# Performance work log

Measured on AMD Instinct MI355X. Metric: run time of the kernel, lower is better.

The kernel has to match this reference:

```python
import jax, jax.numpy as jnp
import numpy as np

POS_MARGIN = 0.01
NEG_MARGIN = 0.2
REG_WEIGHT = 0.1
N, D = 8192, 256
NUM_CLASSES = 512


def setup_inputs() -> dict:
    key = jax.random.key(0)
    k1, k2 = jax.random.split(key)
    embeds = jax.random.normal(k1, (N, D), dtype=jnp.float32)
    labels = jax.random.randint(k2, (N,), 0, NUM_CLASSES, dtype=jnp.int64)
    return {"embeds": embeds, "labels": labels}


def reference(embeds, labels):
    n, d = embeds.shape
    # L2-normalize embeddings (normalize_embeds=True)
    e = embeds / jnp.linalg.norm(embeds, axis=1, keepdims=True)

    # var(e_i - e_j, ddof=1) over feature dim, computed without the [N,N,D] tensor:
    # var = (D/(D-1)) * ( mean(e_i^2) + mean(e_j^2) - 2*mean(e_i*e_j) - (m_i - m_j)^2 )
    m = e.mean(axis=1)                      # [N]
    s = (e * e).mean(axis=1)                # [N]
    g = (e @ e.T) / d                       # [N,N] = mean(e_i * e_j) over D
    corr = d / (d - 1.0)
    var_diff = corr * (s[:, None] + s[None, :] - 2.0 * g - (m[:, None] - m[None, :]) ** 2)
    row_var = corr * (s - m * m)            # torch.var(e, dim=1), unbiased
    distmat = var_diff / row_var[:, None]

    same = labels[:, None] == labels[None, :]
    eye = jnp.eye(n, dtype=bool)
    pos_mask = same & (~eye)                # all same-label pairs (anchor != positive)
    neg_mask = ~same                        # all diff-label pairs

    pos_l = jax.nn.relu(distmat - POS_MARGIN) * pos_mask
    neg_l = jax.nn.relu(NEG_MARGIN - distmat) * neg_mask

    # avg_nonzero_only=True: sum / (# strictly-positive entries + 1e-12)
    pos_loss = pos_l.sum() / ((pos_l > 0).sum().astype(jnp.float32) + 1e-12)
    neg_loss = neg_l.sum() / ((neg_l > 0).sum().astype(jnp.float32) + 1e-12)

    loss = pos_loss + neg_loss
    loss = loss + jnp.abs(e.sum(axis=1)).mean() * REG_WEIGHT
    return loss
```

## Files before the change

kernel.cpp:

```cpp
#include <hip/hip_runtime.h>
#include <hip/hip_bf16.h>

#define NROWS 8192
#define DDIM 256
#define BT 128
#define BK 64
#define GT (NROWS / BT)
#define NBT (GT * (GT + 1) / 2)

using bf16x8 = __attribute__((ext_vector_type(8))) __bf16;
using f32x4  = __attribute__((ext_vector_type(4))) float;

__device__ __forceinline__ void glds16(const unsigned short* g, unsigned short* l) {
    __builtin_amdgcn_global_load_lds(
        (const __attribute__((address_space(1))) unsigned int*)g,
        (__attribute__((address_space(3))) unsigned int*)l,
        16, 0, 0);
}

__device__ __forceinline__ unsigned short f2bf(float f) {
    unsigned int b = __float_as_uint(f);
    unsigned int r = b + 0x7fffu + ((b >> 16) & 1u);
    return (unsigned short)(r >> 16);
}

__global__ __launch_bounds__(256) void rowstats_kernel(
    const float* __restrict__ x, unsigned short* __restrict__ ebf,
    float* __restrict__ aA, float* __restrict__ dA,
    float* __restrict__ bA, float* __restrict__ m2A,
    float* __restrict__ rabs)
{
    int wave = threadIdx.x >> 6;
    int lane = threadIdx.x & 63;
    int row  = blockIdx.x * 4 + wave;

    const float4 v = reinterpret_cast<const float4*>(x + (size_t)row * DDIM)[lane];
    float ss = v.x * v.x + v.y * v.y + v.z * v.z + v.w * v.w;
    float sm = v.x + v.y + v.z + v.w;
    #pragma unroll
    for (int off = 32; off >= 1; off >>= 1) {
        ss += __shfl_xor(ss, off);
        sm += __shfl_xor(sm, off);
    }
    float invn = 1.0f / sqrtf(ss);

    ushort4 o;
    o.x = f2bf(v.x * invn);
    o.y = f2bf(v.y * invn);
    o.z = f2bf(v.z * invn);
    o.w = f2bf(v.w * invn);
    reinterpret_cast<ushort4*>(ebf + (size_t)row * DDIM)[lane] = o;

    if (lane == 0) {
        float Se  = sm * invn;
        float Se2 = ss * invn * invn;
        float m = Se * (1.0f / DDIM);
        float s = Se2 * (1.0f / DDIM);
        float b = s - m * m;
        float a = 1.0f / b;
        aA[row]  = a;
        dA[row]  = a * m;
        bA[row]  = b;
        m2A[row] = 2.0f * m;
        rabs[row] = fabsf(Se);
    }
}

__global__ __launch_bounds__(256) void snr_gemm_kernel(
    const unsigned short* __restrict__ ebf,
    const float* __restrict__ aA, const float* __restrict__ dA,
    const float* __restrict__ bA, const float* __restrict__ m2A,
    const int* __restrict__ labels,
    float* __restrict__ partials)
{
    __shared__ __align__(16) unsigned short As[BT * BK];
    __shared__ __align__(16) unsigned short Bs[BT * BK];
    __shared__ float sAi[BT], sDi[BT], sBi[BT], sM2i[BT];
    __shared__ float sAj[BT], sDj[BT], sBj[BT], sM2j[BT];
    __shared__ int   sLi[BT], sLj[BT];
    __shared__ float redbuf[4][4];

    int tid  = threadIdx.x;
    int lane = tid & 63;
    int wave = tid >> 6;
    int wr = (wave >> 1) * 64;
    int wc = (wave & 1) * 64;

    int t = blockIdx.x;
    int bi = (int)((2.0f * GT + 1.0f
                    - sqrtf((2.0f * GT + 1.0f) * (2.0f * GT + 1.0f) - 8.0f * (float)t)) * 0.5f);
    while ((bi + 1) * GT - ((bi + 1) * bi) / 2 <= t) ++bi;
    while (bi * GT - (bi * (bi - 1)) / 2 > t) --bi;
    int bj = bi + (t - (bi * GT - (bi * (bi - 1)) / 2));
    int rowBase = bi * BT, colBase = bj * BT;
    bool diag = (bi == bj);

    if (tid < BT) {
        int gi = rowBase + tid;
        sAi[tid] = aA[gi]; sDi[tid] = dA[gi]; sBi[tid] = bA[gi]; sM2i[tid] = m2A[gi];
        sLi[tid] = labels[gi];
    } else {
        int tt = tid - BT;
        int gj = colBase + tt;
        sAj[tt] = aA[gj]; sDj[tt] = dA[gj]; sBj[tt] = bA[gj]; sM2j[tt] = m2A[gj];
        sLj[tt] = labels[gj];
    }

    const unsigned short* gA[4];
    const unsigned short* gB[4];
    unsigned short* lpA[4];
    unsigned short* lpB[4];
    #pragma unroll
    for (int p = 0; p < 4; ++p) {
        int q   = p * 256 + tid;
        int row = q >> 3;
        int kc  = (q & 7) ^ (row & 7);
        gA[p] = ebf + (size_t)(rowBase + row) * DDIM + kc * 8;
        gB[p] = ebf + (size_t)(colBase + row) * DDIM + kc * 8;
        lpA[p] = As + q * 8;
        lpB[p] = Bs + q * 8;
    }

    int mrow = lane & 15;
    int kch  = lane >> 4;
    int offA[4][2], offB[4][2];
    #pragma unroll
    for (int t4 = 0; t4 < 4; ++t4) {
        int rA = wr + t4 * 16 + mrow;
        int rB = wc + t4 * 16 + mrow;
        #pragma unroll
        for (int h = 0; h < 2; ++h) {
            offA[t4][h] = (rA * 8 + ((h * 4 + kch) ^ (rA & 7))) * 8;
            offB[t4][h] = (rB * 8 + ((h * 4 + kch) ^ (rB & 7))) * 8;
        }
    }

    f32x4 acc[4][4];
    #pragma unroll
    for (int a = 0; a < 4; ++a)
        #pragma unroll
        for (int b = 0; b < 4; ++b)
            acc[a][b] = (f32x4){0.f, 0.f, 0.f, 0.f};

    for (int it = 0; it < 4; ++it) {
        #pragma unroll
        for (int p = 0; p < 4; ++p) {
            glds16(gA[p], lpA[p]);
            glds16(gB[p], lpB[p]);
            gA[p] += BK;
            gB[p] += BK;
        }
        asm volatile("s_waitcnt vmcnt(0)" ::: "memory");
        __syncthreads();

        #pragma unroll
        for (int h = 0; h < 2; ++h) {
            bf16x8 aF[4], bF[4];
            #pragma unroll
            for (int t4 = 0; t4 < 4; ++t4) {
                aF[t4] = *reinterpret_cast<const bf16x8*>(As + offA[t4][h]);
                bF[t4] = *reinterpret_cast<const bf16x8*>(Bs + offB[t4][h]);
            }
            #pragma unroll
            for (int ti = 0; ti < 4; ++ti)
                #pragma unroll
                for (int tj = 0; tj < 4; ++tj)
                    acc[ti][tj] = __builtin_amdgcn_mfma_f32_16x16x32_bf16(aF[ti], bF[tj], acc[ti][tj], 0, 0, 0);
        }
        __syncthreads();
    }

    float ps = 0.f, ns = 0.f;
    unsigned int pcw = 0, ncw = 0;
    int subr = (lane >> 4) * 4;
    int cj   = lane & 15;

    float bCj[4], mCj[4], aCj[4], dCj[4];
    int LCj[4];
    #pragma unroll
    for (int tj = 0; tj < 4; ++tj) {
        int lj = wc + tj * 16 + cj;
        bCj[tj] = sBj[lj]; mCj[tj] = sM2j[lj];
        aCj[tj] = sAj[lj]; dCj[tj] = sDj[lj];
        LCj[tj] = sLj[lj];
    }

    if (!diag) {
        #pragma unroll
        for (int ti = 0; ti < 4; ++ti) {
            #pragma unroll
            for (int r = 0; r < 4; ++r) {
                int li = wr + ti * 16 + subr + r;
                float aR = sAi[li], dR = sDi[li], bR = sBi[li], m2R = sM2i[li];
                int LR = sLi[li];
                #pragma unroll
                for (int tj = 0; tj < 4; ++tj) {
                    float g2 = acc[ti][tj][r] * (1.0f / 128.0f);
                    bool same = (LR == LCj[tj]);
                    float dij = fmaf(aR, bCj[tj] - g2, fmaf(dR, mCj[tj], 1.0f));
                    float dji = fmaf(aCj[tj], bR - g2, fmaf(dCj[tj], m2R, 1.0f));
                    float v1 = same ? (dij - 0.01f) : (0.2f - dij);
                    float v2 = same ? (dji - 0.01f) : (0.2f - dji);
                    bool p1 = same && (v1 > 0.f);
                    bool p2 = same && (v2 > 0.f);
                    bool n1 = (!same) && (v1 > 0.f);
                    bool n2 = (!same) && (v2 > 0.f);
                    ps += (p1 ? v1 : 0.f) + (p2 ? v2 : 0.f);
                    ns += (n1 ? v1 : 0.f) + (n2 ? v2 : 0.f);
                    pcw += (unsigned)__popcll(__ballot(p1)) + (unsigned)__popcll(__ballot(p2));
                    ncw += (unsigned)__popcll(__ballot(n1)) + (unsigned)__popcll(__ballot(n2));
                }
            }
        }
    } else {
        #pragma unroll
        for (int ti = 0; ti < 4; ++ti) {
            #pragma unroll
            for (int r = 0; r < 4; ++r) {
                int li = wr + ti * 16 + subr + r;
                float aR = sAi[li], dR = sDi[li];
                int LR = sLi[li];
                #pragma unroll
                for (int tj = 0; tj < 4; ++tj) {
                    int lj = wc + tj * 16 + cj;
                    float g2 = acc[ti][tj][r] * (1.0f / 128.0f);
                    bool same = (LR == LCj[tj]);
                    float dij = fmaf(aR, bCj[tj] - g2, fmaf(dR, mCj[tj], 1.0f));
                    float v1 = same ? (dij - 0.01f) : (0.2f - dij);
                    bool p1 = same && (li != lj) && (v1 > 0.f);
                    bool n1 = (!same) && (v1 > 0.f);
                    ps += p1 ? v1 : 0.f;
                    ns += n1 ? v1 : 0.f;
                    pcw += (unsigned)__popcll(__ballot(p1));
                    ncw += (unsigned)__popcll(__ballot(n1));
                }
            }
        }
    }

    #pragma unroll
    for (int off = 32; off >= 1; off >>= 1) {
        ps += __shfl_down(ps, off);
        ns += __shfl_down(ns, off);
    }
    if (lane == 0) {
        redbuf[wave][0] = ps; redbuf[wave][1] = ns;
        redbuf[wave][2] = (float)pcw; redbuf[wave][3] = (float)ncw;
    }
    __syncthreads();
    if (tid < 4) {
        float v = redbuf[0][tid] + redbuf[1][tid] + redbuf[2][tid] + redbuf[3][tid];
        partials[blockIdx.x * 4 + tid] = v;
    }
}

__global__ __launch_bounds__(256) void finalize_kernel(
    const float* __restrict__ partials, const float* __restrict__ rabs,
    float* __restrict__ out)
{
    int tid = threadIdx.x;
    float s0 = 0, s1 = 0, s2 = 0, s3 = 0, rr = 0;
    for (int i = tid; i < NBT; i += 256) {
        float4 p = reinterpret_cast<const float4*>(partials)[i];
        s0 += p.x; s1 += p.y; s2 += p.z; s3 += p.w;
    }
    for (int i = tid; i < NROWS; i += 256) rr += rabs[i];

    #pragma unroll
    for (int off = 32; off >= 1; off >>= 1) {
        s0 += __shfl_down(s0, off);
        s1 += __shfl_down(s1, off);
        s2 += __shfl_down(s2, off);
        s3 += __shfl_down(s3, off);
        rr += __shfl_down(rr, off);
    }
    __shared__ float red[4][5];
    int wave = tid >> 6, lane = tid & 63;
    if (lane == 0) {
        red[wave][0] = s0; red[wave][1] = s1; red[wave][2] = s2;
        red[wave][3] = s3; red[wave][4] = rr;
    }
    __syncthreads();
    if (tid == 0) {
        float a0 = 0, a1 = 0, a2 = 0, a3 = 0, a4 = 0;
        #pragma unroll
        for (int w = 0; w < 4; ++w) {
            a0 += red[w][0]; a1 += red[w][1]; a2 += red[w][2];
            a3 += red[w][3]; a4 += red[w][4];
        }
        float pos = a0 / (a2 + 1e-12f);
        float neg = a1 / (a3 + 1e-12f);
        out[0] = pos + neg + a4 * (0.1f / (float)NROWS);
    }
}

extern "C" void kernel_launch(void* const* d_in, const int* in_sizes, int n_in,
                              void* d_out, int out_size, void* d_ws, size_t ws_size,
                              hipStream_t stream) {
    const float* embeds = (const float*)d_in[0];
    const int*   labels = (const int*)d_in[1];
    float* out = (float*)d_out;

    char* ws = (char*)d_ws;
    unsigned short* ebf = (unsigned short*)ws;
    float* aA   = (float*)(ws + (size_t)NROWS * DDIM * 2);
    float* dA   = aA + NROWS;
    float* bA   = dA + NROWS;
    float* m2A  = bA + NROWS;
    float* rabs = m2A + NROWS;
    float* partials = rabs + NROWS;

    rowstats_kernel<<<NROWS / 4, 256, 0, stream>>>(embeds, ebf, aA, dA, bA, m2A, rabs);

    snr_gemm_kernel<<<NBT, 256, 0, stream>>>(ebf, aA, dA, bA, m2A, labels, partials);

    finalize_kernel<<<1, 256, 0, stream>>>(partials, rabs, out);
}
```

Baseline: 127.5 us.

## Mean-center embeddings, drop labels from GEMM epilogue, correct same-label pairs separately

Rowstats now stores mean-centered bf16 embeddings and folds the scale and offset terms into three per-row constants. The GEMM epilogue then treats every pair as a negative, needing one fma, a max and a count per element, with no label compares or ballots. A new per-class kernel recomputes same-label pairs with wave-level dot products, subtracts their negative contribution and adds their positive loss. Diagonal tiles also skip loading the B tile. The cost is an extra launch, a serial per-class pair loop capped at 512 rows per class, and the risk that bf16 dot products in the correction do not match the MFMA results exactly.

```diff
diff --git a/kernel.cpp b/kernel.cpp
--- a/kernel.cpp
+++ b/kernel.cpp
@@ -1,5 +1,4 @@
 #include <hip/hip_runtime.h>
-#include <hip/hip_bf16.h>
 
 #define NROWS 8192
 #define DDIM 256
@@ -7,6 +6,7 @@
 #define BK 64
 #define GT (NROWS / BT)
 #define NBT (GT * (GT + 1) / 2)
+#define NCLS 512
 
 using bf16x8 = __attribute__((ext_vector_type(8))) __bf16;
 using f32x4  = __attribute__((ext_vector_type(4))) float;
@@ -23,12 +23,14 @@
     unsigned int r = b + 0x7fffu + ((b >> 16) & 1u);
     return (unsigned short)(r >> 16);
 }
+__device__ __forceinline__ float bf2f(unsigned short u) {
+    return __uint_as_float((unsigned)u << 16);
+}
 
 __global__ __launch_bounds__(256) void rowstats_kernel(
     const float* __restrict__ x, unsigned short* __restrict__ ebf,
-    float* __restrict__ aA, float* __restrict__ dA,
-    float* __restrict__ bA, float* __restrict__ m2A,
-    float* __restrict__ rabs)
+    float* __restrict__ aP, float* __restrict__ bs,
+    float* __restrict__ cA, float* __restrict__ rabs)
 {
     int wave = threadIdx.x >> 6;
     int lane = threadIdx.x & 63;
@@ -43,42 +45,39 @@
         sm += __shfl_xor(sm, off);
     }
     float invn = 1.0f / sqrtf(ss);
+    float m = sm * invn * (1.0f / DDIM);
 
     ushort4 o;
-    o.x = f2bf(v.x * invn);
-    o.y = f2bf(v.y * invn);
-    o.z = f2bf(v.z * invn);
-    o.w = f2bf(v.w * invn);
+    o.x = f2bf(v.x * invn - m);
+    o.y = f2bf(v.y * invn - m);
+    o.z = f2bf(v.z * invn - m);
+    o.w = f2bf(v.w * invn - m);
     reinterpret_cast<ushort4*>(ebf + (size_t)row * DDIM)[lane] = o;
 
     if (lane == 0) {
-        float Se  = sm * invn;
-        float Se2 = ss * invn * invn;
-        float m = Se * (1.0f / DDIM);
-        float s = Se2 * (1.0f / DDIM);
-        float b = s - m * m;
-        float a = 1.0f / b;
-        aA[row]  = a;
-        dA[row]  = a * m;
-        bA[row]  = b;
-        m2A[row] = 2.0f * m;
-        rabs[row] = fabsf(Se);
+        float s  = ss * invn * invn * (1.0f / DDIM);
+        float b  = s - m * m;
+        float a  = 1.0f / b;
+        float ap = a * (1.0f / 128.0f);
+        float bv = -128.0f * b;
+        aP[row]   = ap;
+        bs[row]   = bv;
+        cA[row]   = fmaf(ap, bv, 0.2f);
+        rabs[row] = fabsf(sm * invn);
     }
 }
 
 __global__ __launch_bounds__(256) void snr_gemm_kernel(
     const unsigned short* __restrict__ ebf,
-    const float* __restrict__ aA, const float* __restrict__ dA,
-    const float* __restrict__ bA, const float* __restrict__ m2A,
-    const int* __restrict__ labels,
+    const float* __restrict__ aP, const float* __restrict__ bs,
+    const float* __restrict__ cA,
     float* __restrict__ partials)
 {
     __shared__ __align__(16) unsigned short As[BT * BK];
     __shared__ __align__(16) unsigned short Bs[BT * BK];
-    __shared__ float sAi[BT], sDi[BT], sBi[BT], sM2i[BT];
-    __shared__ float sAj[BT], sDj[BT], sBj[BT], sM2j[BT];
-    __shared__ int   sLi[BT], sLj[BT];
-    __shared__ float redbuf[4][4];
+    __shared__ float sAPi[BT], sBsi[BT], sCi[BT];
+    __shared__ float sAPj[BT], sBsj[BT], sCj[BT];
+    __shared__ float redbuf[4][2];
 
     int tid  = threadIdx.x;
     int lane = tid & 63;
@@ -97,13 +96,11 @@
 
     if (tid < BT) {
         int gi = rowBase + tid;
-        sAi[tid] = aA[gi]; sDi[tid] = dA[gi]; sBi[tid] = bA[gi]; sM2i[tid] = m2A[gi];
-        sLi[tid] = labels[gi];
+        sAPi[tid] = aP[gi]; sBsi[tid] = bs[gi]; sCi[tid] = cA[gi];
     } else {
         int tt = tid - BT;
         int gj = colBase + tt;
-        sAj[tt] = aA[gj]; sDj[tt] = dA[gj]; sBj[tt] = bA[gj]; sM2j[tt] = m2A[gj];
-        sLj[tt] = labels[gj];
+        sAPj[tt] = aP[gj]; sBsj[tt] = bs[gj]; sCj[tt] = cA[gj];
     }
 
     const unsigned short* gA[4];
@@ -142,13 +139,20 @@
         for (int b = 0; b < 4; ++b)
             acc[a][b] = (f32x4){0.f, 0.f, 0.f, 0.f};
 
+    const unsigned short* Bfrag = diag ? &As[0] : &Bs[0];
+
     for (int it = 0; it < 4; ++it) {
         #pragma unroll
         for (int p = 0; p < 4; ++p) {
             glds16(gA[p], lpA[p]);
-            glds16(gB[p], lpB[p]);
             gA[p] += BK;
-            gB[p] += BK;
+        }
+        if (!diag) {
+            #pragma unroll
+            for (int p = 0; p < 4; ++p) {
+                glds16(gB[p], lpB[p]);
+                gB[p] += BK;
+            }
         }
         asm volatile("s_waitcnt vmcnt(0)" ::: "memory");
         __syncthreads();
@@ -159,7 +163,7 @@
             #pragma unroll
             for (int t4 = 0; t4 < 4; ++t4) {
                 aF[t4] = *reinterpret_cast<const bf16x8*>(As + offA[t4][h]);
-                bF[t4] = *reinterpret_cast<const bf16x8*>(Bs + offB[t4][h]);
+                bF[t4] = *reinterpret_cast<const bf16x8*>(Bfrag + offB[t4][h]);
             }
             #pragma unroll
             for (int ti = 0; ti < 4; ++ti)
@@ -170,69 +174,58 @@
         __syncthreads();
     }
 
-    float ps = 0.f, ns = 0.f;
-    unsigned int pcw = 0, ncw = 0;
     int subr = (lane >> 4) * 4;
     int cj   = lane & 15;
 
-    float bCj[4], mCj[4], aCj[4], dCj[4];
-    int LCj[4];
+    float aPC[4], bsC[4], cC[4];
     #pragma unroll
     for (int tj = 0; tj < 4; ++tj) {
         int lj = wc + tj * 16 + cj;
-        bCj[tj] = sBj[lj]; mCj[tj] = sM2j[lj];
-        aCj[tj] = sAj[lj]; dCj[tj] = sDj[lj];
-        LCj[tj] = sLj[lj];
-    }
+        aPC[tj] = sAPj[lj]; bsC[tj] = sBsj[lj]; cC[tj] = sCj[lj];
+    }
+
+    float S = 0.f;
+    unsigned C = 0u;
 
     if (!diag) {
         #pragma unroll
         for (int ti = 0; ti < 4; ++ti) {
+            float aPR[4], bsR[4], cR[4];
             #pragma unroll
             for (int r = 0; r < 4; ++r) {
                 int li = wr + ti * 16 + subr + r;
-                float aR = sAi[li], dR = sDi[li], bR = sBi[li], m2R = sM2i[li];
-                int LR = sLi[li];
+                aPR[r] = sAPi[li]; bsR[r] = sBsi[li]; cR[r] = sCi[li];
+            }
+            #pragma unroll
+            for (int tj = 0; tj < 4; ++tj) {
                 #pragma unroll
-                for (int tj = 0; tj < 4; ++tj) {
-                    float g2 = acc[ti][tj][r] * (1.0f / 128.0f);
-                    bool same = (LR == LCj[tj]);
-                    float dij = fmaf(aR, bCj[tj] - g2, fmaf(dR, mCj[tj], 1.0f));
-                    float dji = fmaf(aCj[tj], bR - g2, fmaf(dCj[tj], m2R, 1.0f));
-                    float v1 = same ? (dij - 0.01f) : (0.2f - dij);
-                    float v2 = same ? (dji - 0.01f) : (0.2f - dji);
-                    bool p1 = same && (v1 > 0.f);
-                    bool p2 = same && (v2 > 0.f);
-                    bool n1 = (!same) && (v1 > 0.f);
-                    bool n2 = (!same) && (v2 > 0.f);
-                    ps += (p1 ? v1 : 0.f) + (p2 ? v2 : 0.f);
-                    ns += (n1 ? v1 : 0.f) + (n2 ? v2 : 0.f);
-                    pcw += (unsigned)__popcll(__ballot(p1)) + (unsigned)__popcll(__ballot(p2));
-                    ncw += (unsigned)__popcll(__ballot(n1)) + (unsigned)__popcll(__ballot(n2));
+                for (int r = 0; r < 4; ++r) {
+                    float raw = acc[ti][tj][r];
+                    float v1 = fmaf(aPR[r], raw + bsC[tj], cR[r]);
+                    float v2 = fmaf(aPC[tj], raw + bsR[r], cC[tj]);
+                    S += fmaxf(v1, 0.f) + fmaxf(v2, 0.f);
+                    C += (v1 > 0.f);
+                    C += (v2 > 0.f);
                 }
             }
         }
     } else {
         #pragma unroll
         for (int ti = 0; ti < 4; ++ti) {
+            float aPR[4], cR[4];
             #pragma unroll
             for (int r = 0; r < 4; ++r) {
                 int li = wr + ti * 16 + subr + r;
-                float aR = sAi[li], dR = sDi[li];
-                int LR = sLi[li];
+                aPR[r] = sAPi[li]; cR[r] = sCi[li];
+            }
+            #pragma unroll
+            for (int tj = 0; tj < 4; ++tj) {
                 #pragma unroll
-                for (int tj = 0; tj < 4; ++tj) {
-                    int lj = wc + tj * 16 + cj;
-                    float g2 = acc[ti][tj][r] * (1.0f / 128.0f);
-                    bool same = (LR == LCj[tj]);
-                    float dij = fmaf(aR, bCj[tj] - g2, fmaf(dR, mCj[tj], 1.0f));
-                    float v1 = same ? (dij - 0.01f) : (0.2f - dij);
-                    bool p1 = same && (li != lj) && (v1 > 0.f);
-                    bool n1 = (!same) && (v1 > 0.f);
-                    ps += p1 ? v1 : 0.f;
-                    ns += n1 ? v1 : 0.f;
-                    pcw += (unsigned)__popcll(__ballot(p1));
-                    ncw += (unsigned)__popcll(__ballot(n1));
+                for (int r = 0; r < 4; ++r) {
+                    float raw = acc[ti][tj][r];
+                    float v1 = fmaf(aPR[r], raw + bsC[tj], cR[r]);
+                    S += fmaxf(v1, 0.f);
+                    C += (v1 > 0.f);
                 }
             }
         }
@@ -240,57 +233,127 @@
 
     #pragma unroll
     for (int off = 32; off >= 1; off >>= 1) {
-        ps += __shfl_down(ps, off);
-        ns += __shfl_down(ns, off);
-    }
+        S += __shfl_down(S, off);
+        C += __shfl_down(C, off);
+    }
+    if (lane == 0) { redbuf[wave][0] = S; redbuf[wave][1] = (float)C; }
+    __syncthreads();
+    if (tid < 2) {
+        partials[blockIdx.x * 2 + tid] =
+            redbuf[0][tid] + redbuf[1][tid] + redbuf[2][tid] + redbuf[3][tid];
+    }
+}
+
+__global__ __launch_bounds__(256) void corr_kernel(
+    const unsigned short* __restrict__ ebf,
+    const float* __restrict__ aP, const float* __restrict__ bs,
+    const int* __restrict__ labels,
+    float* __restrict__ corr)
+{
+    __shared__ int rowsL[512];
+    __shared__ int cntS;
+    __shared__ float cred[4][4];
+    int tid  = threadIdx.x;
+    int lane = tid & 63;
+    int wave = tid >> 6;
+    int L = blockIdx.x;
+
+    if (tid == 0) cntS = 0;
+    __syncthreads();
+    for (int i = tid; i < NROWS; i += 256)
+        if (labels[i] == L) { int p = atomicAdd(&cntS, 1); if (p < 512) rowsL[p] = i; }
+    __syncthreads();
+    int n = min(cntS, 512);
+    int T = n * (n + 1) / 2;
+
+    float Ssub = 0.f, Spos = 0.f;
+    unsigned Csub = 0u, Cpos = 0u;
+
+    for (int p = wave; p < T; p += 4) {
+        int r1 = (int)((sqrtf(8.0f * (float)p + 1.0f) - 1.0f) * 0.5f);
+        while ((r1 + 1) * (r1 + 2) / 2 <= p) ++r1;
+        while (r1 * (r1 + 1) / 2 > p) --r1;
+        int c = p - r1 * (r1 + 1) / 2;
+        int u = rowsL[r1], v = rowsL[c];
+
+        ushort4 eu = reinterpret_cast<const ushort4*>(ebf + (size_t)u * DDIM)[lane];
+        ushort4 ev = reinterpret_cast<const ushort4*>(ebf + (size_t)v * DDIM)[lane];
+        float dot = bf2f(eu.x) * bf2f(ev.x) + bf2f(eu.y) * bf2f(ev.y)
+                  + bf2f(eu.z) * bf2f(ev.z) + bf2f(eu.w) * bf2f(ev.w);
+        #pragma unroll
+        for (int off = 32; off >= 1; off >>= 1) dot += __shfl_xor(dot, off);
+
+        if (lane == 0) {
+            float raw = dot + bs[u] + bs[v];
+            float vn1 = fmaf(aP[u], raw, 0.2f);
+            if (u == v) {
+                Ssub += fmaxf(vn1, 0.f); Csub += (vn1 > 0.f);
+            } else {
+                float vn2 = fmaf(aP[v], raw, 0.2f);
+                Ssub += fmaxf(vn1, 0.f) + fmaxf(vn2, 0.f);
+                Csub += (vn1 > 0.f); Csub += (vn2 > 0.f);
+                float vp1 = fmaf(-aP[u], raw, -0.01f);
+                float vp2 = fmaf(-aP[v], raw, -0.01f);
+                Spos += fmaxf(vp1, 0.f) + fmaxf(vp2, 0.f);
+                Cpos += (vp1 > 0.f); Cpos += (vp2 > 0.f);
+            }
+        }
+    }
+
     if (lane == 0) {
-        redbuf[wave][0] = ps; redbuf[wave][1] = ns;
-        redbuf[wave][2] = (float)pcw; redbuf[wave][3] = (float)ncw;
+        cred[wave][0] = Ssub; cred[wave][1] = (float)Csub;
+        cred[wave][2] = Spos; cred[wave][3] = (float)Cpos;
     }
     __syncthreads();
     if (tid < 4) {
-        float v = redbuf[0][tid] + redbuf[1][tid] + redbuf[2][tid] + redbuf[3][tid];
-        partials[blockIdx.x * 4 + tid] = v;
+        corr[L * 4 + tid] = cred[0][tid] + cred[1][tid] + cred[2][tid] + cred[3][tid];
     }
 }
 
 __global__ __launch_bounds__(256) void finalize_kernel(
-    const float* __restrict__ partials, const float* __restrict__ rabs,
-    float* __restrict__ out)
+    const float* __restrict__ partials, const float* __restrict__ corr,
+    const float* __restrict__ rabs, float* __restrict__ out)
 {
     int tid = threadIdx.x;
-    float s0 = 0, s1 = 0, s2 = 0, s3 = 0, rr = 0;
+    float sAll = 0, cAll = 0, sSub = 0, cSub = 0, sPos = 0, cPos = 0, rr = 0;
     for (int i = tid; i < NBT; i += 256) {
-        float4 p = reinterpret_cast<const float4*>(partials)[i];
-        s0 += p.x; s1 += p.y; s2 += p.z; s3 += p.w;
+        float2 p = reinterpret_cast<const float2*>(partials)[i];
+        sAll += p.x; cAll += p.y;
+    }
+    for (int i = tid; i < NCLS; i += 256) {
+        float4 q = reinterpret_cast<const float4*>(corr)[i];
+        sSub += q.x; cSub += q.y; sPos += q.z; cPos += q.w;
     }
     for (int i = tid; i < NROWS; i += 256) rr += rabs[i];
 
     #pragma unroll
     for (int off = 32; off >= 1; off >>= 1) {
-        s0 += __shfl_down(s0, off);
-        s1 += __shfl_down(s1, off);
-        s2 += __shfl_down(s2, off);
-        s3 += __shfl_down(s3, off);
-        rr += __shfl_down(rr, off);
-    }
-    __shared__ float red[4][5];
+        sAll += __shfl_down(sAll, off);
+        cAll += __shfl_down(cAll, off);
+        sSub += __shfl_down(sSub, off);
+        cSub += __shfl_down(cSub, off);
+        sPos += __shfl_down(sPos, off);
+        cPos += __shfl_down(cPos, off);
+        rr   += __shfl_down(rr, off);
+    }
+    __shared__ float red[4][7];
     int wave = tid >> 6, lane = tid & 63;
     if (lane == 0) {
-        red[wave][0] = s0; red[wave][1] = s1; red[wave][2] = s2;
-        red[wave][3] = s3; red[wave][4] = rr;
+        red[wave][0] = sAll; red[wave][1] = cAll; red[wave][2] = sSub;
+        red[wave][3] = cSub; red[wave][4] = sPos; red[wave][5] = cPos;
+        red[wave][6] = rr;
     }
     __syncthreads();
     if (tid == 0) {
-        float a0 = 0, a1 = 0, a2 = 0, a3 = 0, a4 = 0;
-        #pragma unroll
-        for (int w = 0; w < 4; ++w) {
-            a0 += red[w][0]; a1 += red[w][1]; a2 += red[w][2];
-            a3 += red[w][3]; a4 += red[w][4];
-        }
-        float pos = a0 / (a2 + 1e-12f);
-        float neg = a1 / (a3 + 1e-12f);
-        out[0] = pos + neg + a4 * (0.1f / (float)NROWS);
+        float a[7];
+        #pragma unroll
+        for (int k = 0; k < 7; ++k)
+            a[k] = red[0][k] + red[1][k] + red[2][k] + red[3][k];
+        float Sn = a[0] - a[2];
+        float Cn = a[1] - a[3];
+        float pos = (a[5] > 0.5f) ? a[4] / (a[5] + 1e-12f) : 0.0f;
+        float neg = (Cn  > 0.5f) ? Sn   / (Cn  + 1e-12f) : 0.0f;
+        out[0] = pos + neg + a[6] * (0.1f / (float)NROWS);
     }
 }
 
@@ -303,16 +366,18 @@
 
     char* ws = (char*)d_ws;
     unsigned short* ebf = (unsigned short*)ws;
-    float* aA   = (float*)(ws + (size_t)NROWS * DDIM * 2);
-    float* dA   = aA + NROWS;
-    float* bA   = dA + NROWS;
-    float* m2A  = bA + NROWS;
-    float* rabs = m2A + NROWS;
+    float* aP   = (float*)(ws + (size_t)NROWS * DDIM * 2);
+    float* bs   = aP + NROWS;
+    float* cA   = bs + NROWS;
+    float* rabs = cA + NROWS;
     float* partials = rabs + NROWS;
-
-    rowstats_kernel<<<NROWS / 4, 256, 0, stream>>>(embeds, ebf, aA, dA, bA, m2A, rabs);
-
-    snr_gemm_kernel<<<NBT, 256, 0, stream>>>(ebf, aA, dA, bA, m2A, labels, partials);
-
-    finalize_kernel<<<1, 256, 0, stream>>>(partials, rabs, out);
-}
+    float* corr = partials + (size_t)NBT * 2;
+
+    rowstats_kernel<<<NROWS / 4, 256, 0, stream>>>(embeds, ebf, aP, bs, cA, rabs);
+
+    corr_kernel<<<NCLS, 256, 0, stream>>>(ebf, aP, bs, labels, corr);
+
+    snr_gemm_kernel<<<NBT, 256, 0, stream>>>(ebf, aP, bs, cA, partials);
+
+    finalize_kernel<<<1, 256, 0, stream>>>(partials, corr, rabs, out);
+}
```

New measurement: 212.0 us. 1.66x slower.

## Mean-center embeddings and restructure epilogue around negative-loss default with same-label correction

Applied to the files above, without the earlier changes.

Rows are stored mean-centered in bf16, so the GEMM directly yields covariance and the per-pair distance reduces to one add and one FMA with precomputed per-row constants. The epilogue now treats every pair as negative, accumulating relu sums and counts without ballots. It then subtracts the same-label contribution and adds the positive term inside a wave-uniform branch that runs only when some lane has a matching label. This is meant to cut ALU and ballot/popcount work in the epilogue. It relies on cancellation (S minus Ssub), which may add float rounding error, and the finalize step guards against zero counts.

```diff
diff --git a/kernel.cpp b/kernel.cpp
--- a/kernel.cpp
+++ b/kernel.cpp
@@ -1,5 +1,4 @@
 #include <hip/hip_runtime.h>
-#include <hip/hip_bf16.h>
 
 #define NROWS 8192
 #define DDIM 256
@@ -26,9 +25,8 @@
 
 __global__ __launch_bounds__(256) void rowstats_kernel(
     const float* __restrict__ x, unsigned short* __restrict__ ebf,
-    float* __restrict__ aA, float* __restrict__ dA,
-    float* __restrict__ bA, float* __restrict__ m2A,
-    float* __restrict__ rabs)
+    float* __restrict__ aP, float* __restrict__ bs,
+    float* __restrict__ cA, float* __restrict__ rabs)
 {
     int wave = threadIdx.x >> 6;
     int lane = threadIdx.x & 63;
@@ -43,40 +41,38 @@
         sm += __shfl_xor(sm, off);
     }
     float invn = 1.0f / sqrtf(ss);
+    float m = sm * invn * (1.0f / DDIM);
 
     ushort4 o;
-    o.x = f2bf(v.x * invn);
-    o.y = f2bf(v.y * invn);
-    o.z = f2bf(v.z * invn);
-    o.w = f2bf(v.w * invn);
+    o.x = f2bf(v.x * invn - m);
+    o.y = f2bf(v.y * invn - m);
+    o.z = f2bf(v.z * invn - m);
+    o.w = f2bf(v.w * invn - m);
     reinterpret_cast<ushort4*>(ebf + (size_t)row * DDIM)[lane] = o;
 
     if (lane == 0) {
-        float Se  = sm * invn;
-        float Se2 = ss * invn * invn;
-        float m = Se * (1.0f / DDIM);
-        float s = Se2 * (1.0f / DDIM);
-        float b = s - m * m;
-        float a = 1.0f / b;
-        aA[row]  = a;
-        dA[row]  = a * m;
-        bA[row]  = b;
-        m2A[row] = 2.0f * m;
-        rabs[row] = fabsf(Se);
+        float s  = ss * invn * invn * (1.0f / DDIM);
+        float b  = s - m * m;
+        float a  = 1.0f / b;
+        float ap = a * (1.0f / 128.0f);
+        float bv = -128.0f * b;
+        aP[row]   = ap;
+        bs[row]   = bv;
+        cA[row]   = fmaf(ap, bv, 0.2f);
+        rabs[row] = fabsf(sm * invn);
     }
 }
 
 __global__ __launch_bounds__(256) void snr_gemm_kernel(
     const unsigned short* __restrict__ ebf,
-    const float* __restrict__ aA, const float* __restrict__ dA,
-    const float* __restrict__ bA, const float* __restrict__ m2A,
-    const int* __restrict__ labels,
+    const float* __restrict__ aP, const float* __restrict__ bs,
+    const float* __restrict__ cA, const int* __restrict__ labels,
     float* __restrict__ partials)
 {
     __shared__ __align__(16) unsigned short As[BT * BK];
     __shared__ __align__(16) unsigned short Bs[BT * BK];
-    __shared__ float sAi[BT], sDi[BT], sBi[BT], sM2i[BT];
-    __shared__ float sAj[BT], sDj[BT], sBj[BT], sM2j[BT];
+    __shared__ float sAPi[BT], sBsi[BT], sCi[BT];
+    __shared__ float sAPj[BT], sBsj[BT], sCj[BT];
     __shared__ int   sLi[BT], sLj[BT];
     __shared__ float redbuf[4][4];
 
@@ -97,12 +93,12 @@
 
     if (tid < BT) {
         int gi = rowBase + tid;
-        sAi[tid] = aA[gi]; sDi[tid] = dA[gi]; sBi[tid] = bA[gi]; sM2i[tid] = m2A[gi];
+        sAPi[tid] = aP[gi]; sBsi[tid] = bs[gi]; sCi[tid] = cA[gi];
         sLi[tid] = labels[gi];
     } else {
         int tt = tid - BT;
         int gj = colBase + tt;
-        sAj[tt] = aA[gj]; sDj[tt] = dA[gj]; sBj[tt] = bA[gj]; sM2j[tt] = m2A[gj];
+        sAPj[tt] = aP[gj]; sBsj[tt] = bs[gj]; sCj[tt] = cA[gj];
         sLj[tt] = labels[gj];
     }
 
@@ -170,20 +166,20 @@
         __syncthreads();
     }
 
-    float ps = 0.f, ns = 0.f;
-    unsigned int pcw = 0, ncw = 0;
     int subr = (lane >> 4) * 4;
     int cj   = lane & 15;
 
-    float bCj[4], mCj[4], aCj[4], dCj[4];
+    float aPC[4], bsC[4], cC[4];
     int LCj[4];
     #pragma unroll
     for (int tj = 0; tj < 4; ++tj) {
         int lj = wc + tj * 16 + cj;
-        bCj[tj] = sBj[lj]; mCj[tj] = sM2j[lj];
-        aCj[tj] = sAj[lj]; dCj[tj] = sDj[lj];
+        aPC[tj] = sAPj[lj]; bsC[tj] = sBsj[lj]; cC[tj] = sCj[lj];
         LCj[tj] = sLj[lj];
     }
+
+    float S = 0.f, Ssub = 0.f, Spos = 0.f;
+    unsigned C = 0u, Csub = 0u, Cpos = 0u;
 
     if (!diag) {
         #pragma unroll
@@ -191,24 +187,25 @@
             #pragma unroll
             for (int r = 0; r < 4; ++r) {
                 int li = wr + ti * 16 + subr + r;
-                float aR = sAi[li], dR = sDi[li], bR = sBi[li], m2R = sM2i[li];
+                float aR = sAPi[li], bR = sBsi[li], cR = sCi[li];
                 int LR = sLi[li];
                 #pragma unroll
                 for (int tj = 0; tj < 4; ++tj) {
-                    float g2 = acc[ti][tj][r] * (1.0f / 128.0f);
+                    float raw = acc[ti][tj][r];
+                    float v1 = fmaf(aR, raw + bsC[tj], cR);
+                    float v2 = fmaf(aPC[tj], raw + bR, cC[tj]);
+                    S += fmaxf(v1, 0.f) + fmaxf(v2, 0.f);
+                    C += (v1 > 0.f);
+                    C += (v2 > 0.f);
                     bool same = (LR == LCj[tj]);
-                    float dij = fmaf(aR, bCj[tj] - g2, fmaf(dR, mCj[tj], 1.0f));
-                    float dji = fmaf(aCj[tj], bR - g2, fmaf(dCj[tj], m2R, 1.0f));
-                    float v1 = same ? (dij - 0.01f) : (0.2f - dij);
-                    float v2 = same ? (dji - 0.01f) : (0.2f - dji);
-                    bool p1 = same && (v1 > 0.f);
-                    bool p2 = same && (v2 > 0.f);
-                    bool n1 = (!same) && (v1 > 0.f);
-                    bool n2 = (!same) && (v2 > 0.f);
-                    ps += (p1 ? v1 : 0.f) + (p2 ? v2 : 0.f);
-                    ns += (n1 ? v1 : 0.f) + (n2 ? v2 : 0.f);
-                    pcw += (unsigned)__popcll(__ballot(p1)) + (unsigned)__popcll(__ballot(p2));
-                    ncw += (unsigned)__popcll(__ballot(n1)) + (unsigned)__popcll(__ballot(n2));
+                    if (__ballot(same)) {
+                        Ssub += same ? fmaxf(v1, 0.f) + fmaxf(v2, 0.f) : 0.f;
+                        Csub += same ? (unsigned)(v1 > 0.f) + (unsigned)(v2 > 0.f) : 0u;
+                        float vp1 = 0.19f - v1;
+                        float vp2 = 0.19f - v2;
+                        Spos += same ? fmaxf(vp1, 0.f) + fmaxf(vp2, 0.f) : 0.f;
+                        Cpos += same ? (unsigned)(vp1 > 0.f) + (unsigned)(vp2 > 0.f) : 0u;
+                    }
                 }
             }
         }
@@ -218,39 +215,49 @@
             #pragma unroll
             for (int r = 0; r < 4; ++r) {
                 int li = wr + ti * 16 + subr + r;
-                float aR = sAi[li], dR = sDi[li];
+                float aR = sAPi[li], cR = sCi[li];
                 int LR = sLi[li];
                 #pragma unroll
                 for (int tj = 0; tj < 4; ++tj) {
-                    int lj = wc + tj * 16 + cj;
-                    float g2 = acc[ti][tj][r] * (1.0f / 128.0f);
+                    float raw = acc[ti][tj][r];
+                    float v1 = fmaf(aR, raw + bsC[tj], cR);
+                    S += fmaxf(v1, 0.f);
+                    C += (v1 > 0.f);
                     bool same = (LR == LCj[tj]);
-                    float dij = fmaf(aR, bCj[tj] - g2, fmaf(dR, mCj[tj], 1.0f));
-                    float v1 = same ? (dij - 0.01f) : (0.2f - dij);
-                    bool p1 = same && (li != lj) && (v1 > 0.f);
-                    bool n1 = (!same) && (v1 > 0.f);
-                    ps += p1 ? v1 : 0.f;
-                    ns += n1 ? v1 : 0.f;
-                    pcw += (unsigned)__popcll(__ballot(p1));
-                    ncw += (unsigned)__popcll(__ballot(n1));
+                    if (__ballot(same)) {
+                        Ssub += same ? fmaxf(v1, 0.f) : 0.f;
+                        Csub += same ? (unsigned)(v1 > 0.f) : 0u;
+                        int lj = wc + tj * 16 + cj;
+                        bool offd = same && (li != lj);
+                        float vp1 = 0.19f - v1;
+                        Spos += offd ? fmaxf(vp1, 0.f) : 0.f;
+                        Cpos += offd ? (unsigned)(vp1 > 0.f) : 0u;
+                    }
                 }
             }
         }
     }
 
+    float Sn = S - Ssub;
+    float Cn = (float)C - (float)Csub;
+    float Sp = Spos;
+    float Cp = (float)Cpos;
+
     #pragma unroll
     for (int off = 32; off >= 1; off >>= 1) {
-        ps += __shfl_down(ps, off);
-        ns += __shfl_down(ns, off);
+        Sn += __shfl_down(Sn, off);
+        Cn += __shfl_down(Cn, off);
+        Sp += __shfl_down(Sp, off);
+        Cp += __shfl_down(Cp, off);
     }
     if (lane == 0) {
-        redbuf[wave][0] = ps; redbuf[wave][1] = ns;
-        redbuf[wave][2] = (float)pcw; redbuf[wave][3] = (float)ncw;
+        redbuf[wave][0] = Sn; redbuf[wave][1] = Cn;
+        redbuf[wave][2] = Sp; redbuf[wave][3] = Cp;
     }
     __syncthreads();
     if (tid < 4) {
-        float v = redbuf[0][tid] + redbuf[1][tid] + redbuf[2][tid] + redbuf[3][tid];
-        partials[blockIdx.x * 4 + tid] = v;
+        partials[blockIdx.x * 4 + tid] =
+            redbuf[0][tid] + redbuf[1][tid] + redbuf[2][tid] + redbuf[3][tid];
     }
 }
 
@@ -288,8 +295,8 @@
             a0 += red[w][0]; a1 += red[w][1]; a2 += red[w][2];
             a3 += red[w][3]; a4 += red[w][4];
         }
-        float pos = a0 / (a2 + 1e-12f);
-        float neg = a1 / (a3 + 1e-12f);
+        float neg = (a1 > 0.5f) ? a0 / (a1 + 1e-12f) : 0.0f;
+        float pos = (a3 > 0.5f) ? a2 / (a3 + 1e-12f) : 0.0f;
         out[0] = pos + neg + a4 * (0.1f / (float)NROWS);
     }
 }
@@ -303,16 +310,15 @@
 
     char* ws = (char*)d_ws;
     unsigned short* ebf = (unsigned short*)ws;
-    float* aA   = (float*)(ws + (size_t)NROWS * DDIM * 2);
-    float* dA   = aA + NROWS;
-    float* bA   = dA + NROWS;
-    float* m2A  = bA + NROWS;
-    float* rabs = m2A + NROWS;
+    float* aP   = (float*)(ws + (size_t)NROWS * DDIM * 2);
+    float* bs   = aP + NROWS;
+    float* cA   = bs + NROWS;
+    float* rabs = cA + NROWS;
     float* partials = rabs + NROWS;
 
-    rowstats_kernel<<<NROWS / 4, 256, 0, stream>>>(embeds, ebf, aA, dA, bA, m2A, rabs);
-
-    snr_gemm_kernel<<<NBT, 256, 0, stream>>>(ebf, aA, dA, bA, m2A, labels, partials);
+    rowstats_kernel<<<NROWS / 4, 256, 0, stream>>>(embeds, ebf, aP, bs, cA, rabs);
+
+    snr_gemm_kernel<<<NBT, 256, 0, stream>>>(ebf, aP, bs, cA, labels, partials);
 
     finalize_kernel<<<1, 256, 0, stream>>>(partials, rabs, out);
 }
```

Result: slower. 146.8 us (+15.2%).
